# Kernel optimization log

Measured on AMD Instinct MI355X. Metric: run time of the kernel, lower is better.

## Reference

```python
import jax, jax.numpy as jnp
import numpy as np

F_FD = 16      # fdfilter
XLEN = 128     # grid side
BS, CH = 16, 4


def _conv(x, w):
    # x: [N, Cin, H, W], w: [Cout, Cin, kh, kw], VALID, stride 1
    return jax.lax.conv_general_dilated(
        x, w, window_strides=(1, 1), padding='VALID',
        dimension_numbers=('NCHW', 'OIHW', 'NCHW'))


def setup_inputs() -> dict:
    key = jax.random.key(0)
    ks = jax.random.split(key, 14)
    s = 0.1
    F = F_FD
    inp = {
        'xInput': jax.random.normal(ks[0], (BS, CH, XLEN, XLEN), dtype=jnp.float32),
        'wX1':  jax.random.normal(ks[1],  (F, 1, 1, 3), dtype=jnp.float32) * s,
        'wX1L': jax.random.normal(ks[2],  (F, 1, 1, 2), dtype=jnp.float32) * s,
        'wX1R': jax.random.normal(ks[3],  (F, 1, 1, 2), dtype=jnp.float32) * s,
        'wY1':  jax.random.normal(ks[4],  (F, 1, 3, 1), dtype=jnp.float32) * s,
        'wY1L': jax.random.normal(ks[5],  (F, 1, 2, 1), dtype=jnp.float32) * s,
        'wY1R': jax.random.normal(ks[6],  (F, 1, 2, 1), dtype=jnp.float32) * s,
        'wX2':  jax.random.normal(ks[7],  (F, F, 1, 3), dtype=jnp.float32) * s,
        'wX2L': jax.random.normal(ks[8],  (F, F, 1, 2), dtype=jnp.float32) * s,
        'wX2R': jax.random.normal(ks[9],  (F, F, 1, 2), dtype=jnp.float32) * s,
        'wY2':  jax.random.normal(ks[10], (F, F, 3, 1), dtype=jnp.float32) * s,
        'wY2L': jax.random.normal(ks[11], (F, F, 2, 1), dtype=jnp.float32) * s,
        'wY2R': jax.random.normal(ks[12], (F, F, 2, 1), dtype=jnp.float32) * s,
        'wfc':  jax.random.normal(ks[13], (1, 4 * F), dtype=jnp.float32) * s,
        'fdblock': 8,
    }
    return inp


def reference(xInput, wX1, wX1L, wX1R, wY1, wY1L, wY1R,
              wX2, wX2L, wX2R, wY2, wY2L, wY2R, wfc, fdblock):
    BS_, C_, H, W = xInput.shape
    x = xInput.reshape(-1, 1, H, W)  # fold channels into batch, Cin=1
    for _ in range(fdblock):
        # first-order x/y finite-difference stencils with boundary convs
        dX = jnp.concatenate([_conv(x[:, :, :, :2], wX1L),
                              _conv(x, wX1),
                              _conv(x[:, :, :, -2:], wX1R)], axis=3)
        dY = jnp.concatenate([_conv(x[:, :, :2, :], wY1L),
                              _conv(x, wY1),
                              _conv(x[:, :, -2:, :], wY1R)], axis=2)
        # second-order stencils on the first-order fields
        dX2 = jnp.concatenate([_conv(dX[:, :, :, :2], wX2L),
                               _conv(dX, wX2),
                               _conv(dX[:, :, :, -2:], wX2R)], axis=3)
        dY2 = jnp.concatenate([_conv(dY[:, :, :2, :], wY2L),
                               _conv(dY, wY2),
                               _conv(dY[:, :, -2:, :], wY2R)], axis=2)
        combine = jnp.concatenate([dX, dY, dX2, dY2], axis=1)  # [N, 4F, H, W]
        # fc over channel dim (transpose(1,3)+Linear+transpose(1,3) == channel contraction)
        deviation = jnp.einsum('nchw,oc->nohw', combine, wfc)  # [N, 1, H, W]
        x = x + deviation
    return x.reshape(BS_, C_, H, W)
```

## Files before the change

kernel.cpp:

```cpp
#include <hip/hip_runtime.h>

#define F 16
#define XL 128


__device__ __forceinline__ float g1f(const float* __restrict__ w1,
                                     const float* __restrict__ w1L,
                                     const float* __restrict__ w1R,
                                     int f, int v, int wp) {
  if (v == 0) {
    if (wp == 0) return w1L[f * 2 + 0];
    if (wp == 1) return w1L[f * 2 + 1];
    return 0.f;
  }
  if (v == XL - 1) {
    if (wp == XL - 2) return w1R[f * 2 + 0];
    if (wp == XL - 1) return w1R[f * 2 + 1];
    return 0.f;
  }
  int k = wp - (v - 1);
  return (k >= 0 && k < 3) ? w1[f * 3 + k] : 0.f;
}

__global__ __launch_bounds__(256)
void build_bands_kernel(const float* __restrict__ wX1, const float* __restrict__ wX1L,
                        const float* __restrict__ wX1R, const float* __restrict__ wY1,
                        const float* __restrict__ wY1L, const float* __restrict__ wY1R,
                        const float* __restrict__ wX2, const float* __restrict__ wX2L,
                        const float* __restrict__ wX2R, const float* __restrict__ wY2,
                        const float* __restrict__ wY2L, const float* __restrict__ wY2R,
                        const float* __restrict__ wfc, float* __restrict__ bands) {
  __shared__ float r1s[2][3], r1Ls[2][2], r1Rs[2][2];
  __shared__ float qs[2][F][3], qLs[2][F][2], qRs[2][F][2];

  const int t = threadIdx.x;
  if (t < 6) {
    int p = t / 3, k = t % 3;
    const float* w1 = p ? wY1 : wX1;
    int off = p ? F : 0;
    float s = 0.f;
    for (int f = 0; f < F; ++f) s += wfc[off + f] * w1[f * 3 + k];
    r1s[p][k] = s;
  } else if (t < 10) {
    int t2 = t - 6; int p = t2 / 2, k = t2 % 2;
    const float* w1L = p ? wY1L : wX1L;
    int off = p ? F : 0;
    float s = 0.f;
    for (int f = 0; f < F; ++f) s += wfc[off + f] * w1L[f * 2 + k];
    r1Ls[p][k] = s;
  } else if (t < 14) {
    int t2 = t - 10; int p = t2 / 2, k = t2 % 2;
    const float* w1R = p ? wY1R : wX1R;
    int off = p ? F : 0;
    float s = 0.f;
    for (int f = 0; f < F; ++f) s += wfc[off + f] * w1R[f * 2 + k];
    r1Rs[p][k] = s;
  } else if (t < 14 + 96) {
    int t2 = t - 14; int p = t2 / 48; int r = t2 % 48; int fi = r / 3, k = r % 3;
    const float* w2 = p ? wY2 : wX2;
    int off = p ? 3 * F : 2 * F;
    float s = 0.f;
    for (int fo = 0; fo < F; ++fo) s += wfc[off + fo] * w2[(fo * F + fi) * 3 + k];
    qs[p][fi][k] = s;
  } else if (t < 110 + 64) {
    int t2 = t - 110; int p = t2 / 32; int r = t2 % 32; int fi = r / 2, k = r % 2;
    const float* w2L = p ? wY2L : wX2L;
    int off = p ? 3 * F : 2 * F;
    float s = 0.f;
    for (int fo = 0; fo < F; ++fo) s += wfc[off + fo] * w2L[(fo * F + fi) * 2 + k];
    qLs[p][fi][k] = s;
  } else if (t < 174 + 64) {
    int t2 = t - 174; int p = t2 / 32; int r = t2 % 32; int fi = r / 2, k = r % 2;
    const float* w2R = p ? wY2R : wX2R;
    int off = p ? 3 * F : 2 * F;
    float s = 0.f;
    for (int fo = 0; fo < F; ++fo) s += wfc[off + fo] * w2R[(fo * F + fi) * 2 + k];
    qRs[p][fi][k] = s;
  }
  __syncthreads();

  int gid = blockIdx.x * 256 + t;
  if (gid >= 2 * XL * 5) return;
  const int p = gid / (XL * 5);
  const int rem = gid % (XL * 5);
  const int w = rem / 5;
  const int d = rem % 5;
  const int wp = w + d - 2;

  const float* w1  = p ? wY1  : wX1;
  const float* w1L = p ? wY1L : wX1L;
  const float* w1R = p ? wY1R : wX1R;

  float c = 0.f;
  if (wp >= 0 && wp < XL) {
    if (w == 0) {
      if (wp == 0)       c += r1Ls[p][0];
      else if (wp == 1)  c += r1Ls[p][1];
    } else if (w == XL - 1) {
      if (wp == XL - 2)      c += r1Rs[p][0];
      else if (wp == XL - 1) c += r1Rs[p][1];
    } else {
      int k = wp - (w - 1);
      if (k >= 0 && k < 3) c += r1s[p][k];
    }
    if (w == 0) {
      for (int vi = 0; vi < 2; ++vi)
        for (int fi = 0; fi < F; ++fi)
          c += qLs[p][fi][vi] * g1f(w1, w1L, w1R, fi, vi, wp);
    } else if (w == XL - 1) {
      for (int vi = 0; vi < 2; ++vi)
        for (int fi = 0; fi < F; ++fi)
          c += qRs[p][fi][vi] * g1f(w1, w1L, w1R, fi, XL - 2 + vi, wp);
    } else {
      for (int k2 = 0; k2 < 3; ++k2) {
        int v = w - 1 + k2;
        for (int fi = 0; fi < F; ++fi)
          c += qs[p][fi][k2] * g1f(w1, w1L, w1R, fi, v, wp);
      }
    }
  }
  bands[(p * 5 + d) * XL + w] = c;
}

__global__ __launch_bounds__(256)
void fd_main_kernel(const float* __restrict__ x_in, const float* __restrict__ bands,
                    const int* __restrict__ fdp, float* __restrict__ x_out) {
  __shared__ float buf[2][64 * XL];
  __shared__ float cbl[5 * XL];

  const int tid = threadIdx.x;
  const int n = blockIdx.x >> 2;
  const int s = blockIdx.x & 3;
  const int g0 = (s == 0) ? 0 : (s == 1) ? 16 : (s == 2) ? 48 : 64;
  const int l0 = (s == 0) ? 0 : (s == 3) ? 32 : 16;

  if (tid < XL) {
#pragma unroll
    for (int d = 0; d < 5; ++d) cbl[d * XL + tid] = bands[(5 + d) * XL + tid];
  }

  {
    const float4* sg4 = (const float4*)(x_in + n * (XL * XL) + g0 * XL);
    float4* b4 = (float4*)buf[0];
#pragma unroll
    for (int i = 0; i < 8; ++i) b4[tid + 256 * i] = sg4[tid + 256 * i];
  }

  const int p = tid & 63;
  const int rg = tid >> 6;
  const int rbase = rg << 4;
  const int pm = (p > 0) ? p - 1 : 0;
  const int pp = (p < 63) ? p + 1 : 63;

  const float2* bp2 = (const float2*)bands;
  const float2 rb0 = bp2[0 * 64 + p];
  const float2 rb1 = bp2[1 * 64 + p];
  const float2 rb2 = bp2[2 * 64 + p];
  const float2 rb3 = bp2[3 * 64 + p];
  const float2 rb4 = bp2[4 * 64 + p];
  const float cbi0 = bands[(5 + 0) * XL + 64];
  const float cbi1 = bands[(5 + 1) * XL + 64];
  const float cbi2 = bands[(5 + 2) * XL + 64];
  const float cbi3 = bands[(5 + 3) * XL + 64];
  const float cbi4 = bands[(5 + 4) * XL + 64];

  const int fdb = fdp[0];
  float2* out2 = (float2*)(x_out + n * (XL * XL));

  __syncthreads();

  if (fdb == 0) {
    const float2* bc = (const float2*)buf[0];
#pragma unroll
    for (int j = 0; j < 16; ++j) {
      const int r = rbase + j;
      const int lr = r - l0;
      if (lr >= 0 && lr < 32) out2[(32 * s + lr) * 64 + p] = bc[r * 64 + p];
    }
    return;
  }

  for (int t = 0; t < fdb; ++t) {
    const float2* bc = (const float2*)buf[t & 1];
    float2* bn = (float2*)buf[(t & 1) ^ 1];
    const bool last = (t == fdb - 1);

    float2 c_m2 = bc[((rbase >= 2) ? rbase - 2 : 0) * 64 + p];
    float2 c_m1 = bc[((rbase >= 1) ? rbase - 1 : 0) * 64 + p];
    float2 c_0  = bc[(rbase + 0) * 64 + p];
    float2 c_p1 = bc[(rbase + 1) * 64 + p];
    float2 c_p2 = bc[(rbase + 2) * 64 + p];

#pragma unroll
    for (int j = 0; j < 16; ++j) {
      const int r = rbase + j;
      const int gh = g0 + r;
      const float2 hl = bc[r * 64 + pm];
      const float2 hr = bc[r * 64 + pp];
      float b0 = cbi0, b1 = cbi1, b2 = cbi2, b3 = cbi3, b4 = cbi4;
      if (gh < 2 || gh > 125) {
        b0 = cbl[0 * XL + gh]; b1 = cbl[1 * XL + gh]; b2 = cbl[2 * XL + gh];
        b3 = cbl[3 * XL + gh]; b4 = cbl[4 * XL + gh];
      }
      float a0 = c_0.x
        + rb0.x * hl.x  + rb1.x * hl.y  + rb2.x * c_0.x + rb3.x * c_0.y + rb4.x * hr.x
        + b0 * c_m2.x + b1 * c_m1.x + b2 * c_0.x + b3 * c_p1.x + b4 * c_p2.x;
      float a1 = c_0.y
        + rb0.y * hl.y  + rb1.y * c_0.x + rb2.y * c_0.y + rb3.y * hr.x  + rb4.y * hr.y
        + b0 * c_m2.y + b1 * c_m1.y + b2 * c_0.y + b3 * c_p1.y + b4 * c_p2.y;

      if (!last) {
        bn[r * 64 + p] = make_float2(a0, a1);
      } else {
        const int lr = r - l0;
        if (lr >= 0 && lr < 32) out2[(32 * s + lr) * 64 + p] = make_float2(a0, a1);
      }
      c_m2 = c_m1; c_m1 = c_0; c_0 = c_p1; c_p1 = c_p2;
      const int rn = (r + 3 <= 63) ? r + 3 : 63;
      c_p2 = bc[rn * 64 + p];
    }
    if (!last) __syncthreads();
  }
}

extern "C" void kernel_launch(void* const* d_in, const int* in_sizes, int n_in,
                              void* d_out, int out_size, void* d_ws, size_t ws_size,
                              hipStream_t stream) {
  const float* xInput = (const float*)d_in[0];
  const float* wX1  = (const float*)d_in[1];
  const float* wX1L = (const float*)d_in[2];
  const float* wX1R = (const float*)d_in[3];
  const float* wY1  = (const float*)d_in[4];
  const float* wY1L = (const float*)d_in[5];
  const float* wY1R = (const float*)d_in[6];
  const float* wX2  = (const float*)d_in[7];
  const float* wX2L = (const float*)d_in[8];
  const float* wX2R = (const float*)d_in[9];
  const float* wY2  = (const float*)d_in[10];
  const float* wY2L = (const float*)d_in[11];
  const float* wY2R = (const float*)d_in[12];
  const float* wfc  = (const float*)d_in[13];
  const int*   fdp  = (const int*)d_in[14];

  float* bands = (float*)d_ws;
  float* out = (float*)d_out;

  build_bands_kernel<<<5, 256, 0, stream>>>(wX1, wX1L, wX1R, wY1, wY1L, wY1R,
                                            wX2, wX2L, wX2R, wY2, wY2L, wY2R,
                                            wfc, bands);
  fd_main_kernel<<<256, 256, 0, stream>>>(xInput, bands, fdp, out);
}
```

Baseline: 110.1 us.

## Fuse band construction into main stencil kernel with 512 threads and float4 rows

Removes the separate band-building kernel launch: every block now recomputes the folded stencil band coefficients into shared memory before running the iterations. The main loop switches from 256 threads handling float2 columns over 16 rows to 512 threads handling float4 columns over 4 rows, raising parallelism per block and shortening each thread's serial row chain. The cost is redundant band computation in all 256 blocks, including the serial 16-term reductions, and more register pressure from the wider per-thread vectors.

```diff
diff --git a/kernel.cpp b/kernel.cpp
--- a/kernel.cpp
+++ b/kernel.cpp
@@ -22,111 +22,21 @@
   return (k >= 0 && k < 3) ? w1[f * 3 + k] : 0.f;
 }
 
-__global__ __launch_bounds__(256)
-void build_bands_kernel(const float* __restrict__ wX1, const float* __restrict__ wX1L,
-                        const float* __restrict__ wX1R, const float* __restrict__ wY1,
-                        const float* __restrict__ wY1L, const float* __restrict__ wY1R,
-                        const float* __restrict__ wX2, const float* __restrict__ wX2L,
-                        const float* __restrict__ wX2R, const float* __restrict__ wY2,
-                        const float* __restrict__ wY2L, const float* __restrict__ wY2R,
-                        const float* __restrict__ wfc, float* __restrict__ bands) {
+__global__ __launch_bounds__(512)
+void fd_fused_kernel(const float* __restrict__ x_in,
+                     const float* __restrict__ wX1, const float* __restrict__ wX1L,
+                     const float* __restrict__ wX1R, const float* __restrict__ wY1,
+                     const float* __restrict__ wY1L, const float* __restrict__ wY1R,
+                     const float* __restrict__ wX2, const float* __restrict__ wX2L,
+                     const float* __restrict__ wX2R, const float* __restrict__ wY2,
+                     const float* __restrict__ wY2L, const float* __restrict__ wY2R,
+                     const float* __restrict__ wfc, const int* __restrict__ fdp,
+                     float* __restrict__ x_out) {
+  __shared__ __align__(16) float buf[2][64 * XL];
+  __shared__ __align__(16) float rbl[5][XL];
+  __shared__ __align__(16) float cbl[5][XL];
   __shared__ float r1s[2][3], r1Ls[2][2], r1Rs[2][2];
   __shared__ float qs[2][F][3], qLs[2][F][2], qRs[2][F][2];
-
-  const int t = threadIdx.x;
-  if (t < 6) {
-    int p = t / 3, k = t % 3;
-    const float* w1 = p ? wY1 : wX1;
-    int off = p ? F : 0;
-    float s = 0.f;
-    for (int f = 0; f < F; ++f) s += wfc[off + f] * w1[f * 3 + k];
-    r1s[p][k] = s;
-  } else if (t < 10) {
-    int t2 = t - 6; int p = t2 / 2, k = t2 % 2;
-    const float* w1L = p ? wY1L : wX1L;
-    int off = p ? F : 0;
-    float s = 0.f;
-    for (int f = 0; f < F; ++f) s += wfc[off + f] * w1L[f * 2 + k];
-    r1Ls[p][k] = s;
-  } else if (t < 14) {
-    int t2 = t - 10; int p = t2 / 2, k = t2 % 2;
-    const float* w1R = p ? wY1R : wX1R;
-    int off = p ? F : 0;
-    float s = 0.f;
-    for (int f = 0; f < F; ++f) s += wfc[off + f] * w1R[f * 2 + k];
-    r1Rs[p][k] = s;
-  } else if (t < 14 + 96) {
-    int t2 = t - 14; int p = t2 / 48; int r = t2 % 48; int fi = r / 3, k = r % 3;
-    const float* w2 = p ? wY2 : wX2;
-    int off = p ? 3 * F : 2 * F;
-    float s = 0.f;
-    for (int fo = 0; fo < F; ++fo) s += wfc[off + fo] * w2[(fo * F + fi) * 3 + k];
-    qs[p][fi][k] = s;
-  } else if (t < 110 + 64) {
-    int t2 = t - 110; int p = t2 / 32; int r = t2 % 32; int fi = r / 2, k = r % 2;
-    const float* w2L = p ? wY2L : wX2L;
-    int off = p ? 3 * F : 2 * F;
-    float s = 0.f;
-    for (int fo = 0; fo < F; ++fo) s += wfc[off + fo] * w2L[(fo * F + fi) * 2 + k];
-    qLs[p][fi][k] = s;
-  } else if (t < 174 + 64) {
-    int t2 = t - 174; int p = t2 / 32; int r = t2 % 32; int fi = r / 2, k = r % 2;
-    const float* w2R = p ? wY2R : wX2R;
-    int off = p ? 3 * F : 2 * F;
-    float s = 0.f;
-    for (int fo = 0; fo < F; ++fo) s += wfc[off + fo] * w2R[(fo * F + fi) * 2 + k];
-    qRs[p][fi][k] = s;
-  }
-  __syncthreads();
-
-  int gid = blockIdx.x * 256 + t;
-  if (gid >= 2 * XL * 5) return;
-  const int p = gid / (XL * 5);
-  const int rem = gid % (XL * 5);
-  const int w = rem / 5;
-  const int d = rem % 5;
-  const int wp = w + d - 2;
-
-  const float* w1  = p ? wY1  : wX1;
-  const float* w1L = p ? wY1L : wX1L;
-  const float* w1R = p ? wY1R : wX1R;
-
-  float c = 0.f;
-  if (wp >= 0 && wp < XL) {
-    if (w == 0) {
-      if (wp == 0)       c += r1Ls[p][0];
-      else if (wp == 1)  c += r1Ls[p][1];
-    } else if (w == XL - 1) {
-      if (wp == XL - 2)      c += r1Rs[p][0];
-      else if (wp == XL - 1) c += r1Rs[p][1];
-    } else {
-      int k = wp - (w - 1);
-      if (k >= 0 && k < 3) c += r1s[p][k];
-    }
-    if (w == 0) {
-      for (int vi = 0; vi < 2; ++vi)
-        for (int fi = 0; fi < F; ++fi)
-          c += qLs[p][fi][vi] * g1f(w1, w1L, w1R, fi, vi, wp);
-    } else if (w == XL - 1) {
-      for (int vi = 0; vi < 2; ++vi)
-        for (int fi = 0; fi < F; ++fi)
-          c += qRs[p][fi][vi] * g1f(w1, w1L, w1R, fi, XL - 2 + vi, wp);
-    } else {
-      for (int k2 = 0; k2 < 3; ++k2) {
-        int v = w - 1 + k2;
-        for (int fi = 0; fi < F; ++fi)
-          c += qs[p][fi][k2] * g1f(w1, w1L, w1R, fi, v, wp);
-      }
-    }
-  }
-  bands[(p * 5 + d) * XL + w] = c;
-}
-
-__global__ __launch_bounds__(256)
-void fd_main_kernel(const float* __restrict__ x_in, const float* __restrict__ bands,
-                    const int* __restrict__ fdp, float* __restrict__ x_out) {
-  __shared__ float buf[2][64 * XL];
-  __shared__ float cbl[5 * XL];
 
   const int tid = threadIdx.x;
   const int n = blockIdx.x >> 2;
@@ -134,90 +44,178 @@
   const int g0 = (s == 0) ? 0 : (s == 1) ? 16 : (s == 2) ? 48 : 64;
   const int l0 = (s == 0) ? 0 : (s == 3) ? 32 : 16;
 
-  if (tid < XL) {
-#pragma unroll
-    for (int d = 0; d < 5; ++d) cbl[d * XL + tid] = bands[(5 + d) * XL + tid];
-  }
-
   {
     const float4* sg4 = (const float4*)(x_in + n * (XL * XL) + g0 * XL);
     float4* b4 = (float4*)buf[0];
 #pragma unroll
-    for (int i = 0; i < 8; ++i) b4[tid + 256 * i] = sg4[tid + 256 * i];
-  }
-
-  const int p = tid & 63;
-  const int rg = tid >> 6;
-  const int rbase = rg << 4;
-  const int pm = (p > 0) ? p - 1 : 0;
-  const int pp = (p < 63) ? p + 1 : 63;
-
-  const float2* bp2 = (const float2*)bands;
-  const float2 rb0 = bp2[0 * 64 + p];
-  const float2 rb1 = bp2[1 * 64 + p];
-  const float2 rb2 = bp2[2 * 64 + p];
-  const float2 rb3 = bp2[3 * 64 + p];
-  const float2 rb4 = bp2[4 * 64 + p];
-  const float cbi0 = bands[(5 + 0) * XL + 64];
-  const float cbi1 = bands[(5 + 1) * XL + 64];
-  const float cbi2 = bands[(5 + 2) * XL + 64];
-  const float cbi3 = bands[(5 + 3) * XL + 64];
-  const float cbi4 = bands[(5 + 4) * XL + 64];
+    for (int i = 0; i < 4; ++i) b4[tid + 512 * i] = sg4[tid + 512 * i];
+  }
+
+  {
+    const int t = tid;
+    if (t < 6) {
+      int p = t / 3, k = t % 3;
+      const float* w1 = p ? wY1 : wX1;
+      int off = p ? F : 0;
+      float sm = 0.f;
+      for (int f = 0; f < F; ++f) sm += wfc[off + f] * w1[f * 3 + k];
+      r1s[p][k] = sm;
+    } else if (t < 10) {
+      int t2 = t - 6; int p = t2 / 2, k = t2 % 2;
+      const float* w1L = p ? wY1L : wX1L;
+      int off = p ? F : 0;
+      float sm = 0.f;
+      for (int f = 0; f < F; ++f) sm += wfc[off + f] * w1L[f * 2 + k];
+      r1Ls[p][k] = sm;
+    } else if (t < 14) {
+      int t2 = t - 10; int p = t2 / 2, k = t2 % 2;
+      const float* w1R = p ? wY1R : wX1R;
+      int off = p ? F : 0;
+      float sm = 0.f;
+      for (int f = 0; f < F; ++f) sm += wfc[off + f] * w1R[f * 2 + k];
+      r1Rs[p][k] = sm;
+    } else if (t < 14 + 96) {
+      int t2 = t - 14; int p = t2 / 48; int r = t2 % 48; int fi = r / 3, k = r % 3;
+      const float* w2 = p ? wY2 : wX2;
+      int off = p ? 3 * F : 2 * F;
+      float sm = 0.f;
+      for (int fo = 0; fo < F; ++fo) sm += wfc[off + fo] * w2[(fo * F + fi) * 3 + k];
+      qs[p][fi][k] = sm;
+    } else if (t < 110 + 64) {
+      int t2 = t - 110; int p = t2 / 32; int r = t2 % 32; int fi = r / 2, k = r % 2;
+      const float* w2L = p ? wY2L : wX2L;
+      int off = p ? 3 * F : 2 * F;
+      float sm = 0.f;
+      for (int fo = 0; fo < F; ++fo) sm += wfc[off + fo] * w2L[(fo * F + fi) * 2 + k];
+      qLs[p][fi][k] = sm;
+    } else if (t < 174 + 64) {
+      int t2 = t - 174; int p = t2 / 32; int r = t2 % 32; int fi = r / 2, k = r % 2;
+      const float* w2R = p ? wY2R : wX2R;
+      int off = p ? 3 * F : 2 * F;
+      float sm = 0.f;
+      for (int fo = 0; fo < F; ++fo) sm += wfc[off + fo] * w2R[(fo * F + fi) * 2 + k];
+      qRs[p][fi][k] = sm;
+    }
+  }
+  __syncthreads();
+
+  for (int e = tid; e < 2 * 5 * XL; e += 512) {
+    const int pp = e / (5 * XL);
+    const int rem = e % (5 * XL);
+    const int w = rem / 5;
+    const int d = rem % 5;
+    const int wp = w + d - 2;
+    const float* w1  = pp ? wY1  : wX1;
+    const float* w1L = pp ? wY1L : wX1L;
+    const float* w1R = pp ? wY1R : wX1R;
+    float c = 0.f;
+    if (wp >= 0 && wp < XL) {
+      if (w == 0) {
+        if (wp == 0)       c += r1Ls[pp][0];
+        else if (wp == 1)  c += r1Ls[pp][1];
+      } else if (w == XL - 1) {
+        if (wp == XL - 2)      c += r1Rs[pp][0];
+        else if (wp == XL - 1) c += r1Rs[pp][1];
+      } else {
+        int k = wp - (w - 1);
+        if (k >= 0 && k < 3) c += r1s[pp][k];
+      }
+      if (w == 0) {
+        for (int vi = 0; vi < 2; ++vi)
+          for (int fi = 0; fi < F; ++fi)
+            c += qLs[pp][fi][vi] * g1f(w1, w1L, w1R, fi, vi, wp);
+      } else if (w == XL - 1) {
+        for (int vi = 0; vi < 2; ++vi)
+          for (int fi = 0; fi < F; ++fi)
+            c += qRs[pp][fi][vi] * g1f(w1, w1L, w1R, fi, XL - 2 + vi, wp);
+      } else {
+        for (int k2 = 0; k2 < 3; ++k2) {
+          int v = w - 1 + k2;
+          for (int fi = 0; fi < F; ++fi)
+            c += qs[pp][fi][k2] * g1f(w1, w1L, w1R, fi, v, wp);
+        }
+      }
+    }
+    if (pp == 0) rbl[d][w] = c; else cbl[d][w] = c;
+  }
+  __syncthreads();
+
+  const int q = tid & 31;
+  const int rbase = (tid >> 5) << 2;
+  const int plm = (q > 0) ? 2 * q - 1 : 0;
+  const int prm = (q < 31) ? 2 * q + 2 : 63;
+
+  const float4 rb0 = ((const float4*)rbl[0])[q];
+  const float4 rb1 = ((const float4*)rbl[1])[q];
+  const float4 rb2 = ((const float4*)rbl[2])[q];
+  const float4 rb3 = ((const float4*)rbl[3])[q];
+  const float4 rb4 = ((const float4*)rbl[4])[q];
+  const float cbi0 = cbl[0][64];
+  const float cbi1 = cbl[1][64];
+  const float cbi2 = cbl[2][64];
+  const float cbi3 = cbl[3][64];
+  const float cbi4 = cbl[4][64];
 
   const int fdb = fdp[0];
-  float2* out2 = (float2*)(x_out + n * (XL * XL));
-
-  __syncthreads();
+  float4* out4 = (float4*)(x_out + n * (XL * XL));
 
   if (fdb == 0) {
-    const float2* bc = (const float2*)buf[0];
+    const float4* bc = (const float4*)buf[0];
 #pragma unroll
-    for (int j = 0; j < 16; ++j) {
+    for (int j = 0; j < 4; ++j) {
       const int r = rbase + j;
       const int lr = r - l0;
-      if (lr >= 0 && lr < 32) out2[(32 * s + lr) * 64 + p] = bc[r * 64 + p];
+      if (lr >= 0 && lr < 32) out4[(32 * s + lr) * 32 + q] = bc[r * 32 + q];
     }
     return;
   }
 
   for (int t = 0; t < fdb; ++t) {
-    const float2* bc = (const float2*)buf[t & 1];
-    float2* bn = (float2*)buf[(t & 1) ^ 1];
+    const float4* bc  = (const float4*)buf[t & 1];
+    const float2* bc2 = (const float2*)buf[t & 1];
+    float4* bn = (float4*)buf[(t & 1) ^ 1];
     const bool last = (t == fdb - 1);
 
-    float2 c_m2 = bc[((rbase >= 2) ? rbase - 2 : 0) * 64 + p];
-    float2 c_m1 = bc[((rbase >= 1) ? rbase - 1 : 0) * 64 + p];
-    float2 c_0  = bc[(rbase + 0) * 64 + p];
-    float2 c_p1 = bc[(rbase + 1) * 64 + p];
-    float2 c_p2 = bc[(rbase + 2) * 64 + p];
+    float4 c_m2 = bc[((rbase >= 2) ? rbase - 2 : 0) * 32 + q];
+    float4 c_m1 = bc[((rbase >= 1) ? rbase - 1 : 0) * 32 + q];
+    float4 c_0  = bc[(rbase + 0) * 32 + q];
+    float4 c_p1 = bc[(rbase + 1) * 32 + q];
+    float4 c_p2 = bc[(rbase + 2) * 32 + q];
 
 #pragma unroll
-    for (int j = 0; j < 16; ++j) {
+    for (int j = 0; j < 4; ++j) {
       const int r = rbase + j;
       const int gh = g0 + r;
-      const float2 hl = bc[r * 64 + pm];
-      const float2 hr = bc[r * 64 + pp];
-      float b0 = cbi0, b1 = cbi1, b2 = cbi2, b3 = cbi3, b4 = cbi4;
+      const float2 hl = bc2[r * 64 + plm];
+      const float2 hr = bc2[r * 64 + prm];
+      float b0 = cbi0, b1 = cbi1, b2 = cbi2, b3 = cbi3, b4c = cbi4;
       if (gh < 2 || gh > 125) {
-        b0 = cbl[0 * XL + gh]; b1 = cbl[1 * XL + gh]; b2 = cbl[2 * XL + gh];
-        b3 = cbl[3 * XL + gh]; b4 = cbl[4 * XL + gh];
-      }
-      float a0 = c_0.x
-        + rb0.x * hl.x  + rb1.x * hl.y  + rb2.x * c_0.x + rb3.x * c_0.y + rb4.x * hr.x
-        + b0 * c_m2.x + b1 * c_m1.x + b2 * c_0.x + b3 * c_p1.x + b4 * c_p2.x;
-      float a1 = c_0.y
-        + rb0.y * hl.y  + rb1.y * c_0.x + rb2.y * c_0.y + rb3.y * hr.x  + rb4.y * hr.y
-        + b0 * c_m2.y + b1 * c_m1.y + b2 * c_0.y + b3 * c_p1.y + b4 * c_p2.y;
+        b0 = cbl[0][gh]; b1 = cbl[1][gh]; b2 = cbl[2][gh];
+        b3 = cbl[3][gh]; b4c = cbl[4][gh];
+      }
+      float4 a;
+      a.x = c_0.x
+        + rb0.x * hl.x  + rb1.x * hl.y  + rb2.x * c_0.x + rb3.x * c_0.y + rb4.x * c_0.z
+        + b0 * c_m2.x + b1 * c_m1.x + b2 * c_0.x + b3 * c_p1.x + b4c * c_p2.x;
+      a.y = c_0.y
+        + rb0.y * hl.y  + rb1.y * c_0.x + rb2.y * c_0.y + rb3.y * c_0.z + rb4.y * c_0.w
+        + b0 * c_m2.y + b1 * c_m1.y + b2 * c_0.y + b3 * c_p1.y + b4c * c_p2.y;
+      a.z = c_0.z
+        + rb0.z * c_0.x + rb1.z * c_0.y + rb2.z * c_0.z + rb3.z * c_0.w + rb4.z * hr.x
+        + b0 * c_m2.z + b1 * c_m1.z + b2 * c_0.z + b3 * c_p1.z + b4c * c_p2.z;
+      a.w = c_0.w
+        + rb0.w * c_0.y + rb1.w * c_0.z + rb2.w * c_0.w + rb3.w * hr.x  + rb4.w * hr.y
+        + b0 * c_m2.w + b1 * c_m1.w + b2 * c_0.w + b3 * c_p1.w + b4c * c_p2.w;
 
       if (!last) {
-        bn[r * 64 + p] = make_float2(a0, a1);
+        bn[r * 32 + q] = a;
       } else {
         const int lr = r - l0;
-        if (lr >= 0 && lr < 32) out2[(32 * s + lr) * 64 + p] = make_float2(a0, a1);
+        if (lr >= 0 && lr < 32) out4[(32 * s + lr) * 32 + q] = a;
       }
       c_m2 = c_m1; c_m1 = c_0; c_0 = c_p1; c_p1 = c_p2;
       const int rn = (r + 3 <= 63) ? r + 3 : 63;
-      c_p2 = bc[rn * 64 + p];
+      c_p2 = bc[rn * 32 + q];
     }
     if (!last) __syncthreads();
   }
@@ -242,11 +240,9 @@
   const float* wfc  = (const float*)d_in[13];
   const int*   fdp  = (const int*)d_in[14];
 
-  float* bands = (float*)d_ws;
   float* out = (float*)d_out;
 
-  build_bands_kernel<<<5, 256, 0, stream>>>(wX1, wX1L, wX1R, wY1, wY1L, wY1R,
-                                            wX2, wX2L, wX2R, wY2, wY2L, wY2R,
-                                            wfc, bands);
-  fd_main_kernel<<<256, 256, 0, stream>>>(xInput, bands, fdp, out);
+  fd_fused_kernel<<<256, 512, 0, stream>>>(xInput, wX1, wX1L, wX1R, wY1, wY1L, wY1R,
+                                           wX2, wX2L, wX2R, wY2, wY2L, wY2R,
+                                           wfc, fdp, out);
 }
```

New measurement: 108.7 us. Within noise of the previous version (-1.3%).

## Split image into 8 row slabs with 48-row halo tiles and float4 lanes

Applied to the files above, without the earlier changes.

Each image is now split into 8 output slabs of 16 rows instead of 4 slabs of 32. Each block loads a 48-row halo tile, so the grid grows to 512 blocks of 512 threads with smaller LDS per block. Each thread now computes 4 columns by 3 rows with float4 shared-memory accesses instead of 2 columns by 16 rows, and the last iteration is peeled into its own call. This should raise occupancy and the number of blocks in flight, at the cost of more redundant halo recompute (48 rows loaded per 16 output).

```diff
diff --git a/kernel.cpp b/kernel.cpp
--- a/kernel.cpp
+++ b/kernel.cpp
@@ -122,42 +122,41 @@
   bands[(p * 5 + d) * XL + w] = c;
 }
 
-__global__ __launch_bounds__(256)
+#define BR 48
+__global__ __launch_bounds__(512, 4)
 void fd_main_kernel(const float* __restrict__ x_in, const float* __restrict__ bands,
                     const int* __restrict__ fdp, float* __restrict__ x_out) {
-  __shared__ float buf[2][64 * XL];
+  __shared__ __align__(16) float buf[2][BR * XL + 512];
   __shared__ float cbl[5 * XL];
 
   const int tid = threadIdx.x;
-  const int n = blockIdx.x >> 2;
-  const int s = blockIdx.x & 3;
-  const int g0 = (s == 0) ? 0 : (s == 1) ? 16 : (s == 2) ? 48 : 64;
-  const int l0 = (s == 0) ? 0 : (s == 3) ? 32 : 16;
-
+  const int n = blockIdx.x >> 3;
+  const int s = blockIdx.x & 7;
+  int g0 = 16 * s - 16; if (g0 < 0) g0 = 0; if (g0 > XL - BR) g0 = XL - BR;
+  const int l0 = 16 * s - g0;
+
+  {
+    const float4* sg4 = (const float4*)(x_in + n * (XL * XL) + g0 * XL);
+    float4* b4 = (float4*)buf[0];
+    b4[tid] = sg4[tid];
+    b4[tid + 512] = sg4[tid + 512];
+    b4[tid + 1024] = sg4[tid + 1024];
+  }
   if (tid < XL) {
 #pragma unroll
     for (int d = 0; d < 5; ++d) cbl[d * XL + tid] = bands[(5 + d) * XL + tid];
   }
 
-  {
-    const float4* sg4 = (const float4*)(x_in + n * (XL * XL) + g0 * XL);
-    float4* b4 = (float4*)buf[0];
-#pragma unroll
-    for (int i = 0; i < 8; ++i) b4[tid + 256 * i] = sg4[tid + 256 * i];
-  }
-
-  const int p = tid & 63;
-  const int rg = tid >> 6;
-  const int rbase = rg << 4;
-  const int pm = (p > 0) ? p - 1 : 0;
-  const int pp = (p < 63) ? p + 1 : 63;
-
-  const float2* bp2 = (const float2*)bands;
-  const float2 rb0 = bp2[0 * 64 + p];
-  const float2 rb1 = bp2[1 * 64 + p];
-  const float2 rb2 = bp2[2 * 64 + p];
-  const float2 rb3 = bp2[3 * 64 + p];
-  const float2 rb4 = bp2[4 * 64 + p];
+  const int q = tid & 31;
+  const int rbase = (tid >> 5) * 3;
+  const int plm = (q > 0) ? 2 * q - 1 : 0;
+  const int prm = (q < 31) ? 2 * q + 2 : 63;
+
+  const float4 rb0 = ((const float4*)(bands + 0 * XL))[q];
+  const float4 rb1 = ((const float4*)(bands + 1 * XL))[q];
+  const float4 rb2 = ((const float4*)(bands + 2 * XL))[q];
+  const float4 rb3 = ((const float4*)(bands + 3 * XL))[q];
+  const float4 rb4 = ((const float4*)(bands + 4 * XL))[q];
   const float cbi0 = bands[(5 + 0) * XL + 64];
   const float cbi1 = bands[(5 + 1) * XL + 64];
   const float cbi2 = bands[(5 + 2) * XL + 64];
@@ -165,62 +164,71 @@
   const float cbi4 = bands[(5 + 4) * XL + 64];
 
   const int fdb = fdp[0];
-  float2* out2 = (float2*)(x_out + n * (XL * XL));
+  float4* out4 = (float4*)(x_out + n * (XL * XL));
 
   __syncthreads();
 
   if (fdb == 0) {
-    const float2* bc = (const float2*)buf[0];
+    const float4* bc = (const float4*)buf[0];
 #pragma unroll
-    for (int j = 0; j < 16; ++j) {
+    for (int j = 0; j < 3; ++j) {
       const int r = rbase + j;
       const int lr = r - l0;
-      if (lr >= 0 && lr < 32) out2[(32 * s + lr) * 64 + p] = bc[r * 64 + p];
+      if (lr >= 0 && lr < 16) out4[(16 * s + lr) * 32 + q] = bc[r * 32 + q];
     }
     return;
   }
 
-  for (int t = 0; t < fdb; ++t) {
-    const float2* bc = (const float2*)buf[t & 1];
-    float2* bn = (float2*)buf[(t & 1) ^ 1];
-    const bool last = (t == fdb - 1);
-
-    float2 c_m2 = bc[((rbase >= 2) ? rbase - 2 : 0) * 64 + p];
-    float2 c_m1 = bc[((rbase >= 1) ? rbase - 1 : 0) * 64 + p];
-    float2 c_0  = bc[(rbase + 0) * 64 + p];
-    float2 c_p1 = bc[(rbase + 1) * 64 + p];
-    float2 c_p2 = bc[(rbase + 2) * 64 + p];
-
+  auto step = [&](const float* bufc, auto&& emit) {
+    const float4* bc  = (const float4*)bufc;
+    const float2* bc2 = (const float2*)bufc;
+    float4 c_m2 = bc[((rbase >= 2) ? rbase - 2 : 0) * 32 + q];
+    float4 c_m1 = bc[((rbase >= 1) ? rbase - 1 : 0) * 32 + q];
+    float4 c_0  = bc[(rbase + 0) * 32 + q];
+    float4 c_p1 = bc[(rbase + 1) * 32 + q];
+    float4 c_p2 = bc[(rbase + 2) * 32 + q];
 #pragma unroll
-    for (int j = 0; j < 16; ++j) {
+    for (int j = 0; j < 3; ++j) {
       const int r = rbase + j;
       const int gh = g0 + r;
-      const float2 hl = bc[r * 64 + pm];
-      const float2 hr = bc[r * 64 + pp];
-      float b0 = cbi0, b1 = cbi1, b2 = cbi2, b3 = cbi3, b4 = cbi4;
+      const float2 hl = bc2[r * 64 + plm];
+      const float2 hr = bc2[r * 64 + prm];
+      float b0 = cbi0, b1 = cbi1, b2 = cbi2, b3 = cbi3, b4c = cbi4;
       if (gh < 2 || gh > 125) {
         b0 = cbl[0 * XL + gh]; b1 = cbl[1 * XL + gh]; b2 = cbl[2 * XL + gh];
-        b3 = cbl[3 * XL + gh]; b4 = cbl[4 * XL + gh];
+        b3 = cbl[3 * XL + gh]; b4c = cbl[4 * XL + gh];
       }
-      float a0 = c_0.x
-        + rb0.x * hl.x  + rb1.x * hl.y  + rb2.x * c_0.x + rb3.x * c_0.y + rb4.x * hr.x
-        + b0 * c_m2.x + b1 * c_m1.x + b2 * c_0.x + b3 * c_p1.x + b4 * c_p2.x;
-      float a1 = c_0.y
-        + rb0.y * hl.y  + rb1.y * c_0.x + rb2.y * c_0.y + rb3.y * hr.x  + rb4.y * hr.y
-        + b0 * c_m2.y + b1 * c_m1.y + b2 * c_0.y + b3 * c_p1.y + b4 * c_p2.y;
-
-      if (!last) {
-        bn[r * 64 + p] = make_float2(a0, a1);
-      } else {
-        const int lr = r - l0;
-        if (lr >= 0 && lr < 32) out2[(32 * s + lr) * 64 + p] = make_float2(a0, a1);
+      float4 a;
+      a.x = c_0.x
+        + rb0.x * hl.x  + rb1.x * hl.y  + rb2.x * c_0.x + rb3.x * c_0.y + rb4.x * c_0.z
+        + b0 * c_m2.x + b1 * c_m1.x + b2 * c_0.x + b3 * c_p1.x + b4c * c_p2.x;
+      a.y = c_0.y
+        + rb0.y * hl.y  + rb1.y * c_0.x + rb2.y * c_0.y + rb3.y * c_0.z + rb4.y * c_0.w
+        + b0 * c_m2.y + b1 * c_m1.y + b2 * c_0.y + b3 * c_p1.y + b4c * c_p2.y;
+      a.z = c_0.z
+        + rb0.z * c_0.x + rb1.z * c_0.y + rb2.z * c_0.z + rb3.z * c_0.w + rb4.z * hr.x
+        + b0 * c_m2.z + b1 * c_m1.z + b2 * c_0.z + b3 * c_p1.z + b4c * c_p2.z;
+      a.w = c_0.w
+        + rb0.w * c_0.y + rb1.w * c_0.z + rb2.w * c_0.w + rb3.w * hr.x  + rb4.w * hr.y
+        + b0 * c_m2.w + b1 * c_m1.w + b2 * c_0.w + b3 * c_p1.w + b4c * c_p2.w;
+      emit(r, a);
+      if (j < 2) {
+        c_m2 = c_m1; c_m1 = c_0; c_0 = c_p1; c_p1 = c_p2;
+        const int rn = (r + 3 <= BR - 1) ? r + 3 : BR - 1;
+        c_p2 = bc[rn * 32 + q];
       }
-      c_m2 = c_m1; c_m1 = c_0; c_0 = c_p1; c_p1 = c_p2;
-      const int rn = (r + 3 <= 63) ? r + 3 : 63;
-      c_p2 = bc[rn * 64 + p];
-    }
-    if (!last) __syncthreads();
-  }
+    }
+  };
+
+  for (int t = 0; t < fdb - 1; ++t) {
+    float4* bn = (float4*)buf[(t & 1) ^ 1];
+    step(buf[t & 1], [&](int r, float4 a) { bn[r * 32 + q] = a; });
+    __syncthreads();
+  }
+  step(buf[(fdb - 1) & 1], [&](int r, float4 a) {
+    const int lr = r - l0;
+    if (lr >= 0 && lr < 16) out4[(16 * s + lr) * 32 + q] = a;
+  });
 }
 
 extern "C" void kernel_launch(void* const* d_in, const int* in_sizes, int n_in,
@@ -248,5 +256,5 @@
   build_bands_kernel<<<5, 256, 0, stream>>>(wX1, wX1L, wX1R, wY1, wY1L, wY1R,
                                             wX2, wX2L, wX2R, wY2, wY2L, wY2R,
                                             wfc, bands);
-  fd_main_kernel<<<256, 256, 0, stream>>>(xInput, bands, fdp, out);
-}
+  fd_main_kernel<<<512, 512, 0, stream>>>(xInput, bands, fdp, out);
+}
```

Result: no change. 110.6 us (+0.5%).
